# Performance work log

Hardware: AMD Instinct MI355X
Metric: run time of the kernel (lower is better)

## Reference

```python
import jax, jax.numpy as jnp
import numpy as np

NEG = -1e9
NP_N, EP = 30000, 480000
NL, EL, T = 48, 144, 96
NA, D = 11, 256
I_STOP = NL
PHI = 1 + 5 * D + 4 * NA
VAL_VEC = jnp.array([4., 1., 3., 1., 2., 1., 5., 1., 6., 1., 1000.], dtype=jnp.float32)
BOND_VAL = jnp.array([1., 2., 3., 1.5], dtype=jnp.float32)


def gcn2(x, src, dst, w, W1, b1, W2, b2):
    # two-layer GCN with symmetric norm + self loops (PyG GCNConv semantics)
    n = x.shape[0]
    loops = jnp.arange(n, dtype=src.dtype)
    s = jnp.concatenate([src, loops])
    d = jnp.concatenate([dst, loops])
    ww = jnp.concatenate([w, jnp.ones((n,), x.dtype)])
    deg = jax.ops.segment_sum(ww, d, num_segments=n)
    dinv = jnp.where(deg > 0, deg ** -0.5, 0.0)
    norm = (ww * dinv[s] * dinv[d])[:, None]
    def conv(h, W, b):
        return jax.ops.segment_sum((h @ W)[s] * norm, d, num_segments=n) + b
    return conv(jax.nn.relu(conv(x, W1, b1)), W2, b2)


def _forward(x_p, x_l_geom, Wp1, bp1, Wp2, bp2, Wl1, bl1, Wl2, bl2,
             Wd1, bd1, Wd2, bd2, Wf, bf, Wg, bg, Wh, bh,
             src_p, dst_p, src_l, dst_l, x_l_label, bfs_index, bfs_bond):
    f32, i32 = jnp.float32, jnp.int32
    src_p = src_p.astype(i32); dst_p = dst_p.astype(i32)
    src_l = src_l.astype(i32); dst_l = dst_l.astype(i32)
    bfs_index = bfs_index.astype(i32); bfs_bond = bfs_bond.astype(i32)
    x_l_label = x_l_label.astype(i32)
    x_l = jnp.concatenate([x_l_geom, jax.nn.one_hot(x_l_label, NA, dtype=f32)], 1)
    z_pocket = gcn2(x_p, src_p, dst_p, jnp.ones((EP,), f32), Wp1, bp1, Wp2, bp2).mean(0)
    z_l = gcn2(x_l, src_l, dst_l, jnp.ones((EL,), f32), Wl1, bl1, Wl2, bl2)
    lab_true = x_l[:, 4:]
    # f: atom label classifier, teacher-forced log prob of true labels
    lmask = jnp.zeros((NA,), f32).at[-1].set(NEG)
    logp = jax.nn.log_softmax(z_l @ Wf + bf + lmask, -1)[jnp.arange(NL), x_l_label].sum()
    H_init = jnp.concatenate([z_l, lab_true], 1).mean(0)
    lab_v = jnp.concatenate([lab_true, jax.nn.one_hot(jnp.array([NA - 1]), NA, dtype=f32)], 0)  # append Stop node
    e0 = bfs_index[0]
    z_v0 = gcn2(lab_v, e0[:1], e0[1:2], jnp.ones((1,), f32), Wd1, bd1, Wd2, bd2)
    H_t0 = jnp.concatenate([z_v0, lab_v], 1).mean(0)
    val0 = lab_v @ VAL_VEC
    N1 = NL + 1
    E = 2 * T
    Q0 = jnp.zeros((T + 1,), i32).at[0].set(bfs_index[0, 0])
    carry0 = (jnp.asarray(0.0, f32), val0, jnp.zeros((N1,), bool), jnp.zeros((N1, N1), bool),
              jnp.zeros((E,), i32), jnp.zeros((E,), i32), jnp.zeros((E,), bool), jnp.asarray(0, i32),
              Q0, jnp.asarray(0, i32), jnp.asarray(1, i32), z_v0, H_t0, jnp.asarray(0.0, f32))

    def step(carry, xs):
        logp, val, closed, adj, esrc, edst, evalid, ec, Q, head, tail, z_v, H_t, time = carry
        v, bidx = xs
        active = tail > head
        u = Q[head]
        phi = jnp.concatenate([
            jnp.full((N1, 1), time, f32),
            jnp.broadcast_to(z_pocket, (N1, D)),
            jnp.broadcast_to(z_v[u], (N1, D)),
            jnp.broadcast_to(lab_v[u], (N1, NA)),
            z_v, lab_v,
            jnp.broadcast_to(H_t, (N1, D + NA)),
            jnp.broadcast_to(H_init, (N1, D + NA))], 1)
        # node mask (valency / closed / already-bonded / self), then unmask {v, stop}
        base = jnp.where((val < 1) | closed | adj[u], NEG, 0.0).at[u].set(NEG)
        m_nou = jnp.where(val[u] < 1, jnp.full((N1,), NEG, f32), base)
        m = m_nou.at[v].set(0.0).at[I_STOP].set(0.0)
        glog = (phi @ Wg + bg)[:, 0] + m
        logp = logp + jnp.where(active, jax.nn.log_softmax(glog)[v], 0.0)
        is_stop = v == I_STOP
        pop = active & is_stop
        do_edge = active & (~is_stop)
        closed = closed.at[u].set(jnp.where(pop, True, closed[u]))
        head = head + pop.astype(jnp.int32)
        Q = Q.at[tail].set(jnp.where(do_edge, v, Q[tail]), mode='drop')
        tail = tail + do_edge.astype(jnp.int32)
        esrc = esrc.at[ec].set(u, mode='drop').at[ec + 1].set(v, mode='drop')
        edst = edst.at[ec].set(v, mode='drop').at[ec + 1].set(u, mode='drop')
        evalid = evalid.at[ec].set(do_edge, mode='drop').at[ec + 1].set(do_edge, mode='drop')
        ec = ec + 2 * do_edge.astype(jnp.int32)
        # bond mask row on min valency of (u, v)
        mv = jnp.minimum(val[u], val[v])
        two = jnp.array([0., 0., NEG, 0.], f32)
        one = jnp.array([0., NEG, NEG, 0.], f32)
        zer = jnp.full((4,), NEG, f32)
        e = jnp.where(mv <= 2, two, jnp.zeros((4,), f32))
        e = jnp.where(mv <= 1, one, e)
        e = jnp.where(mv <= 0, zer, e)
        e = jnp.where(m_nou[v] <= NEG * 0.5, zer, e)
        e = e.at[bidx].set(0.0)  # unmask true bond
        hlog = phi[v] @ Wh + bh + e
        logp = logp + jnp.where(do_edge, jax.nn.log_softmax(hlog)[bidx], 0.0)
        dec = jnp.where(do_edge, BOND_VAL[bidx], 0.0)
        val = val.at[u].add(-dec).at[v].add(-dec)
        adj = adj.at[u, v].set(jnp.where(do_edge, True, adj[u, v])).at[v, u].set(jnp.where(do_edge, True, adj[v, u]))
        z_new = gcn2(lab_v, esrc, edst, evalid.astype(f32), Wd1, bd1, Wd2, bd2)
        z_v = jnp.where(do_edge, z_new, z_v)
        H_t = jnp.where(do_edge, jnp.concatenate([z_new, lab_v], 1).mean(0), H_t)
        time = time + do_edge.astype(f32)
        return (logp, val, closed, adj, esrc, edst, evalid, ec, Q, head, tail, z_v, H_t, time), None

    carry, _ = jax.lax.scan(step, carry0, (bfs_index[:, 1], bfs_bond))
    return carry[0]


def setup_inputs():
    key = jax.random.key(0)
    ks = jax.random.split(key, 30)
    f32 = jnp.float32
    def w(i, shape):
        return jax.random.normal(ks[i], shape, f32) * 0.05
    inp = {}
    inp['x_p'] = jax.random.normal(ks[0], (NP_N, 15), f32)
    inp['src_p'] = jax.random.randint(ks[1], (EP,), 0, NP_N)
    inp['dst_p'] = jax.random.randint(ks[2], (EP,), 0, NP_N)
    inp['x_l_geom'] = jax.random.normal(ks[3], (NL, 4), f32)
    inp['x_l_label'] = jax.random.randint(ks[4], (NL,), 0, NA - 1)
    inp['src_l'] = jax.random.randint(ks[5], (EL,), 0, NL)
    inp['dst_l'] = jax.random.randint(ks[6], (EL,), 0, NL)
    inp['bfs_index'] = jax.random.randint(ks[7], (T, 2), 0, NL + 1)
    inp['bfs_bond'] = jax.random.randint(ks[8], (T,), 0, 4)
    inp['Wp1'] = w(9, (15, D)); inp['bp1'] = w(10, (D,))
    inp['Wp2'] = w(11, (D, D)); inp['bp2'] = w(12, (D,))
    inp['Wl1'] = w(13, (15, D)); inp['bl1'] = w(14, (D,))
    inp['Wl2'] = w(15, (D, D)); inp['bl2'] = w(16, (D,))
    inp['Wd1'] = w(17, (NA, D)); inp['bd1'] = w(18, (D,))
    inp['Wd2'] = w(19, (D, D)); inp['bd2'] = w(20, (D,))
    inp['Wf'] = w(21, (D, NA)); inp['bf'] = w(22, (NA,))
    inp['Wg'] = w(23, (PHI, 1)); inp['bg'] = w(24, (1,))
    inp['Wh'] = w(25, (PHI, 4)); inp['bh'] = w(26, (4,))
    return inp


def reference(x_p, src_p, dst_p, x_l_geom, x_l_label, src_l, dst_l, bfs_index, bfs_bond,
              Wp1, bp1, Wp2, bp2, Wl1, bl1, Wl2, bl2, Wd1, bd1, Wd2, bd2,
              Wf, bf, Wg, bg, Wh, bh):
    return _forward(x_p, x_l_geom, Wp1, bp1, Wp2, bp2, Wl1, bl1, Wl2, bl2,
                    Wd1, bd1, Wd2, bd2, Wf, bf, Wg, bg, Wh, bh,
                    src_p, dst_p, src_l, dst_l, x_l_label, bfs_index, bfs_bond)
```

## Files before the change

### kernel.cpp

```cpp
#include <hip/hip_runtime.h>
#include <math.h>

#define NPn 30000
#define EPn 480000
#define NLl 48
#define ELl 144
#define Tn 96
#define NAn 11
#define Dn 256
#define N1 49
#define NEGf (-1000000000.0f)
#define NSTATES 97
#define CHN 125
#define PC 13
#define YN (N1*PC)


__global__ __launch_bounds__(256) void kA(
    const int* __restrict__ dst_p, int* __restrict__ deg,
    const int* __restrict__ lab_in, const int* __restrict__ bfs_i, const int* __restrict__ bfs_b,
    int* __restrict__ lab_idx, float* __restrict__ lab_means,
    int* __restrict__ dirs, int* __restrict__ dird, float* __restrict__ m_arr,
    float* __restrict__ e_arr, int* __restrict__ rec, int* __restrict__ Sout,
    const float* __restrict__ xg, const int* __restrict__ srcl, const int* __restrict__ dstl,
    const float* __restrict__ Wl1, const float* __restrict__ bl1,
    const float* __restrict__ Wl2, const float* __restrict__ bl2, float* __restrict__ zl_mean,
    const float* __restrict__ Wd2, const float* __restrict__ Wg, const float* __restrict__ Wh,
    float* __restrict__ Pm){
  const int bid = blockIdx.x;
  const int tid = threadIdx.x;

  if (bid == 0){
    __shared__ int sv[Tn], sb[Tn];
    __shared__ int qarr[Tn+1];
    __shared__ int uArr[Tn], headA[Tn], doeA[Tn], popA[Tn], actA[Tn], timeA[Tn], eidxA[Tn];
    __shared__ float decA[Tn], valuA[Tn], valvA[Tn];
    __shared__ float baseB[Tn][N1];
    __shared__ int slab[N1];
    __shared__ int cntL[NAn];
    if (tid < Tn){ sv[tid]=bfs_i[2*tid+1]; sb[tid]=bfs_b[tid]; }
    if (tid <= Tn) qarr[tid]=0;
    if (tid < NAn) cntL[tid]=0;
    if (tid < N1){ int l=(tid<NLl)? lab_in[tid] : (NAn-1); slab[tid]=l; lab_idx[tid]=l; }
    __syncthreads();
    if (tid < NLl) atomicAdd(&cntL[slab[tid]],1);
    if (tid == 0) qarr[0]=bfs_i[0];
    __syncthreads();
    if (tid < NAn){
      int c=cntL[tid];
      lab_means[tid]     = ((float)c + ((tid==NAn-1)?1.f:0.f))*(1.0f/49.0f);
      lab_means[NAn+tid] = (float)c*(1.0f/48.0f);
    }
    if (tid == 0){
      dirs[192]=qarr[0]; dird[192]=bfs_i[1];
      int head=0, tail=1, ec=0, timec=0;
      for (int t=0;t<Tn;t++){
        int v = sv[t];
        int active = (tail>head)?1:0;
        int is_stop = (v==NLl)?1:0;
        int pop = active & is_stop;
        int doe = active & (is_stop^1);
        headA[t]=head; actA[t]=active; doeA[t]=doe; popA[t]=pop; timeA[t]=timec;
        eidxA[t] = doe ? ec : -1;
        int bix = sb[t];
        decA[t] = (bix==0)?1.f:(bix==1)?2.f:(bix==2)?3.f:1.5f;
        if (doe && tail<=Tn) qarr[tail]=v;
        head+=pop; tail+=doe; ec+=2*doe; timec+=doe;
      }
      Sout[0]=ec/2;
    }
    __syncthreads();
    if (tid < Tn){
      int t=tid;
      int h=headA[t]; if (h>Tn) h=Tn;
      int u=qarr[h];
      uArr[t]=u;
      rec[t]=u; rec[Tn+t]=sv[t]; rec[2*Tn+t]=sb[t];
      rec[3*Tn+t]=actA[t]; rec[4*Tn+t]=doeA[t]; rec[5*Tn+t]=timeA[t];
      int ei=eidxA[t];
      if (ei>=0 && ei<192){
        int v=sv[t];
        dirs[ei]=u; dird[ei]=v; dirs[ei+1]=v; dird[ei+1]=u;
      }
    }
    __syncthreads();
    if (tid < 64){
      const int l = tid;
      int labv = (l<N1)? slab[l] : 0;
      float val;
      switch(labv){
        case 0: val=4.f; break; case 1: val=1.f; break; case 2: val=3.f; break;
        case 3: val=1.f; break; case 4: val=2.f; break; case 5: val=1.f; break;
        case 6: val=5.f; break; case 7: val=1.f; break; case 8: val=6.f; break;
        case 9: val=1.f; break; default: val=1000.f; break;
      }
      if (l>=N1) val=0.f;
      int closed=0;
      unsigned long long adjm=0ull;
      for (int t=0;t<Tn;t++){
        int u=uArr[t], v=sv[t];
        int doe=doeA[t], pop=popA[t];
        float base = (val<1.f || closed || ((adjm>>u)&1ull)) ? NEGf : 0.f;
        if (l==u) base=NEGf;
        if (l<N1) baseB[t][l]=base;
        if (l==u) valuA[t]=val;
        if (l==v) valvA[t]=val;
        if (doe){
          float dec=decA[t];
          if (l==u){ val-=dec; adjm |= (1ull<<v); }
          if (l==v){ val-=dec; adjm |= (1ull<<u); }
        }
        if (pop && l==u) closed=1;
      }
    }
    __syncthreads();
    {
      const int lane=tid&63, wv=tid>>6;
      for (int t=wv; t<Tn; t+=4){
        float valu=valuA[t], valv=valvA[t];
        int v=sv[t], bix=sb[t];
        if (lane<N1){
          float mnou = (valu<1.f)? NEGf : baseB[t][lane];
          float m = mnou;
          if (lane==v) m=0.f;
          if (lane==NLl) m=0.f;
          m_arr[t*N1+lane]=m;
        }
        if (lane<4){
          float mnv = (valu<1.f)? NEGf : baseB[t][v];
          float mv = fminf(valu,valv);
          float e;
          if (mv<=0.f) e=NEGf;
          else if (mv<=1.f) e=((lane==1)||(lane==2))?NEGf:0.f;
          else if (mv<=2.f) e=(lane==2)?NEGf:0.f;
          else e=0.f;
          if (mnv <= NEGf*0.5f) e=NEGf;
          if (lane==bix) e=0.f;
          e_arr[t*4+lane]=e;
        }
      }
    }
    return;
  }

  if (bid == 1){
    __shared__ float sW[15*Dn];
    __shared__ float svec[NLl*4];
    __shared__ float scnt[NLl*11];
    __shared__ float ow[NLl];
    __shared__ float rs[Dn];
    __shared__ float sdinv[NLl];
    __shared__ int sdeg[NLl];
    __shared__ int ses[ELl], sed[ELl];
    __shared__ int slab2[NLl];
    if (tid<NLl){ sdeg[tid]=1; slab2[tid]=lab_in[tid]; }
    for (int i=tid;i<NLl*4;i+=256) svec[i]=0.f;
    for (int i=tid;i<NLl*11;i+=256) scnt[i]=0.f;
    for (int i=tid;i<15*Dn;i+=256) sW[i]=Wl1[i];
    __syncthreads();
    if (tid<ELl){ ses[tid]=srcl[tid]; sed[tid]=dstl[tid]; atomicAdd(&sdeg[dstl[tid]],1); }
    __syncthreads();
    if (tid<NLl) sdinv[tid]=rsqrtf((float)sdeg[tid]);
    __syncthreads();
    if (tid<NLl){
      float dv=sdinv[tid];
      ow[tid]=dv;
      for (int q=0;q<4;q++) svec[tid*4+q]=xg[tid*4+q]*dv;
      scnt[tid*11+slab2[tid]]=dv;
    }
    __syncthreads();
    if (tid<ELl){
      int s=ses[tid], d=sed[tid];
      float dvs=sdinv[s];
      for (int q=0;q<4;q++) atomicAdd(&svec[d*4+q], xg[s*4+q]*dvs);
      atomicAdd(&scnt[d*11+slab2[s]], dvs);
      atomicAdd(&ow[s], sdinv[d]);
    }
    __syncthreads();
    {
      int c=tid;
      float b=bl1[c];
      float rsum=0.f;
      for (int d=0;d<NLl;d++){
        float a=0.f;
        for (int q=0;q<4;q++)  a=fmaf(svec[d*4+q], sW[q*Dn+c], a);
        for (int aa=0;aa<11;aa++) a=fmaf(scnt[d*11+aa], sW[(4+aa)*Dn+c], a);
        float h=fmaxf(sdinv[d]*a + b, 0.f);
        rsum = fmaf(sdinv[d]*ow[d], h, rsum);
      }
      rs[c]=rsum*(1.0f/48.0f);
    }
    __syncthreads();
    {
      int c=tid;
      float a=0.f;
      for (int k=0;k<Dn;k++) a=fmaf(rs[k], Wl2[(size_t)k*Dn+c], a);
      zl_mean[c]=a+bl2[c];
    }
    return;
  }

  if (bid < 2+64){
    const int lane = tid&63, wv = tid>>6;
    const int k = (bid-2)*4 + wv;
    float pg=0.f;
    float4 pu=make_float4(0,0,0,0), pv=make_float4(0,0,0,0), ph=make_float4(0,0,0,0);
    for (int q=0;q<4;q++){
      int n = lane + 64*q;
      float w = Wd2[(size_t)k*Dn+n];
      pg = fmaf(w, Wg[524+n], pg);
      float4 a=*(const float4*)&Wh[(size_t)(257+n)*4];
      float4 b=*(const float4*)&Wh[(size_t)(524+n)*4];
      float4 c=*(const float4*)&Wh[(size_t)(791+n)*4];
      pu.x=fmaf(w,a.x,pu.x); pu.y=fmaf(w,a.y,pu.y); pu.z=fmaf(w,a.z,pu.z); pu.w=fmaf(w,a.w,pu.w);
      pv.x=fmaf(w,b.x,pv.x); pv.y=fmaf(w,b.y,pv.y); pv.z=fmaf(w,b.z,pv.z); pv.w=fmaf(w,b.w,pv.w);
      ph.x=fmaf(w,c.x,ph.x); ph.y=fmaf(w,c.y,ph.y); ph.z=fmaf(w,c.z,ph.z); ph.w=fmaf(w,c.w,ph.w);
    }
    for (int off=32; off>0; off>>=1){
      pg += __shfl_xor(pg,off);
      pu.x+=__shfl_xor(pu.x,off); pu.y+=__shfl_xor(pu.y,off); pu.z+=__shfl_xor(pu.z,off); pu.w+=__shfl_xor(pu.w,off);
      pv.x+=__shfl_xor(pv.x,off); pv.y+=__shfl_xor(pv.y,off); pv.z+=__shfl_xor(pv.z,off); pv.w+=__shfl_xor(pv.w,off);
      ph.x+=__shfl_xor(ph.x,off); ph.y+=__shfl_xor(ph.y,off); ph.z+=__shfl_xor(ph.z,off); ph.w+=__shfl_xor(ph.w,off);
    }
    if (lane==0){
      float* o = Pm + k*PC;
      o[0]=pg; o[1]=pu.x; o[2]=pu.y; o[3]=pu.z; o[4]=pu.w;
      o[5]=pv.x; o[6]=pv.y; o[7]=pv.z; o[8]=pv.w;
      o[9]=ph.x; o[10]=ph.y; o[11]=ph.z; o[12]=ph.w;
    }
    return;
  }

  {
    int e = (bid-66)*256 + tid;
    if (e < EPn) atomicAdd(&deg[dst_p[e]], 1);
  }
}


__global__ void k_xagg(const int* __restrict__ src, const int* __restrict__ dst,
                       const float* __restrict__ xp, const int* __restrict__ deg,
                       float* __restrict__ xagg, float* __restrict__ odegw){
  int g = blockIdx.x*blockDim.x + threadIdx.x;
  int e = g>>4, c = g&15;
  if (e >= EPn) return;
  int s = src[e], d = dst[e];
  if (c < 15){
    float dvs = rsqrtf((float)(deg[s]+1));
    atomicAdd(&xagg[d*16+c], xp[s*15+c]*dvs);
  } else {
    float dvd = rsqrtf((float)(deg[d]+1));
    atomicAdd(&odegw[s], dvd);
  }
}

__global__ __launch_bounds__(256) void k_fuse(const float* __restrict__ xp, const float* __restrict__ xagg,
    const int* __restrict__ deg, const float* __restrict__ odegw,
    const float* __restrict__ Wp1, const float* __restrict__ bp1, float* __restrict__ zr){
  __shared__ float sx[CHN][16];
  __shared__ float sc[CHN];
  int tid = threadIdx.x;
  int base = blockIdx.x*CHN;
  float wcol[15];
  for (int k=0;k<15;k++) wcol[k]=Wp1[k*Dn+tid];
  float b = bp1[tid];
  for (int i=tid;i<CHN*16;i+=256){
    int n = base+(i>>4), c = i&15;
    float v = 0.f;
    if (n<NPn && c<15){
      float dv = rsqrtf((float)(deg[n]+1));
      v = (xagg[n*16+c] + xp[n*15+c]*dv)*dv;
    }
    sx[i>>4][i&15]=v;
  }
  for (int i=tid;i<CHN;i+=256){
    int n = base+i;
    float dv = (n<NPn)? rsqrtf((float)(deg[n]+1)) : 0.f;
    sc[i] = (n<NPn)? dv*(odegw[n]+dv) : 0.f;
  }
  __syncthreads();
  float acc = 0.f;
  int lim = (NPn-base < CHN)? (NPn-base) : CHN;
  for (int i=0;i<lim;i++){
    float d0 = b;
    for (int k=0;k<15;k++) d0 = fmaf(sx[i][k], wcol[k], d0);
    acc = fmaf(sc[i], fmaxf(d0,0.f), acc);
  }
  atomicAdd(&zr[tid], acc);
}


__global__ __launch_bounds__(256) void k_zh(const float* __restrict__ zr, const float* __restrict__ Wp2,
    const float* __restrict__ bp2, const float* __restrict__ zl, const float* __restrict__ lm,
    const float* __restrict__ b2, const float* __restrict__ Wh, const float* __restrict__ bh,
    float* __restrict__ hc4){
  __shared__ float sr[Dn];
  __shared__ float zp[Dn];
  int tid=threadIdx.x;
  sr[tid]=zr[tid]*(1.0f/30000.0f);
  __syncthreads();
  float a=0.f;
  for (int k=0;k<Dn;k++) a=fmaf(sr[k],Wp2[(size_t)k*Dn+tid],a);
  zp[tid]=a+bp2[tid];
  __syncthreads();
  if (tid<64){
    int lane=tid;
    float4 h=make_float4(0,0,0,0);
    for (int q=0;q<4;q++){
      int n=lane+64*q;
      float4 w1=*(const float4*)&Wh[(size_t)(1+n)*4];
      float4 w2=*(const float4*)&Wh[(size_t)(1058+n)*4];
      float4 wu=*(const float4*)&Wh[(size_t)(257+n)*4];
      float4 wv=*(const float4*)&Wh[(size_t)(524+n)*4];
      float4 wh=*(const float4*)&Wh[(size_t)(791+n)*4];
      float zpn=zp[n], zln=zl[n], bn=b2[n];
      h.x += zpn*w1.x + zln*w2.x + bn*(wu.x+wv.x+wh.x);
      h.y += zpn*w1.y + zln*w2.y + bn*(wu.y+wv.y+wh.y);
      h.z += zpn*w1.z + zln*w2.z + bn*(wu.z+wv.z+wh.z);
      h.w += zpn*w1.w + zln*w2.w + bn*(wu.w+wv.w+wh.w);
    }
    if (lane<NAn){
      float4 wa=*(const float4*)&Wh[(size_t)(1047+lane)*4];
      float4 wb=*(const float4*)&Wh[(size_t)(1314+lane)*4];
      float aa=lm[lane], bb=lm[NAn+lane];
      h.x += aa*wa.x + bb*wb.x; h.y += aa*wa.y + bb*wb.y;
      h.z += aa*wa.z + bb*wb.z; h.w += aa*wa.w + bb*wb.w;
    }
    for (int off=32; off>0; off>>=1){
      h.x+=__shfl_xor(h.x,off); h.y+=__shfl_xor(h.y,off);
      h.z+=__shfl_xor(h.z,off); h.w+=__shfl_xor(h.w,off);
    }
    if (lane==0){
      hc4[0]=h.x+bh[0]; hc4[1]=h.y+bh[1]; hc4[2]=h.z+bh[2]; hc4[3]=h.w+bh[3];
    }
  }
}


__global__ __launch_bounds__(256) void k_dc(const int* __restrict__ Sp, const int* __restrict__ dirs,
    const int* __restrict__ dird, const int* __restrict__ lab_idx,
    const float* __restrict__ Wd1, const float* __restrict__ bd1,
    const float* __restrict__ Pm, const int* __restrict__ rec,
    const float* __restrict__ m_arr, const float* __restrict__ e_arr,
    const float* __restrict__ hc4, const float* __restrict__ Wg, const float* __restrict__ Wh,
    float* __restrict__ out){
  int k = blockIdx.x;
  if (k > Sp[0]) return;
  __shared__ float sW[11*Dn];
  __shared__ float sP[Dn*PC];
  __shared__ float hT[Dn*N1];
  __shared__ float cnt[N1*11];
  __shared__ float y1[YN];
  __shared__ float za[YN];
  __shared__ float sdinv[N1];
  __shared__ int sdeg[N1];
  __shared__ int se[192], sd[192];
  __shared__ int slab[N1];
  __shared__ int srec[6*Tn];
  int tid=threadIdx.x;
  int ecnt = (k==0)?1:(2*k);
  int base = (k==0)?192:0;
  if (tid<N1){ sdeg[tid]=1; slab[tid]=lab_idx[tid]; }
  for (int i=tid;i<N1*11;i+=256) cnt[i]=0.f;
  for (int i=tid;i<11*Dn;i+=256) sW[i]=Wd1[i];
  for (int i=tid;i<Dn*PC;i+=256) sP[i]=Pm[i];
  for (int i=tid;i<6*Tn;i+=256) srec[i]=rec[i];
  __syncthreads();
  if (tid<ecnt){ se[tid]=dirs[base+tid]; sd[tid]=dird[base+tid]; atomicAdd(&sdeg[sd[tid]],1); }
  __syncthreads();
  if (tid<N1) sdinv[tid]=rsqrtf((float)sdeg[tid]);
  __syncthreads();
  if (tid<N1) cnt[tid*11+slab[tid]] = sdinv[tid];
  __syncthreads();
  if (tid<ecnt) atomicAdd(&cnt[sd[tid]*11+slab[se[tid]]], sdinv[se[tid]]);
  __syncthreads();
  {
    int c=tid;
    float wreg[11];
    for (int a=0;a<11;a++) wreg[a]=sW[a*Dn+c];
    float b=bd1[c];
    for (int r=0;r<N1;r++){
      float s=0.f;
      for (int a=0;a<11;a++) s=fmaf(cnt[r*11+a], wreg[a], s);
      hT[c*N1+r]=fmaxf(sdinv[r]*s + b, 0.f);
    }
  }
  __syncthreads();
  for (int idx=tid; idx<YN; idx+=256){
    int r=idx/PC, j=idx-r*PC;
    float acc=0.f;
    for (int c=0;c<Dn;c++) acc=fmaf(hT[c*N1+r], sP[c*PC+j], acc);
    y1[idx]=acc;
    za[idx]=sdinv[r]*acc;
  }
  __syncthreads();
  for (int i=tid; i<ecnt*PC; i+=256){
    int e=i/PC, j=i-e*PC;
    atomicAdd(&za[sd[e]*PC+j], sdinv[se[e]]*y1[se[e]*PC+j]);
  }
  __syncthreads();
  for (int idx=tid; idx<YN; idx+=256){
    int r=idx/PC;
    za[idx]=sdinv[r]*za[idx];
  }
  __syncthreads();
  if (tid>=64) return;
  const int lane=tid;
  for (int t=0;t<Tn;t++){
    if (!srec[3*Tn+t] || srec[5*Tn+t]!=k) continue;
    const int u=srec[t], v=srec[Tn+t], bidx=srec[2*Tn+t], doe=srec[4*Tn+t];
    float g = -INFINITY;
    float4 hm = make_float4(0,0,0,0);
    if (lane<N1){
      const float* zrow = za + lane*PC;
      g = zrow[0] + Wg[780+slab[lane]] + m_arr[t*N1+lane];
      hm.x=zrow[9]; hm.y=zrow[10]; hm.z=zrow[11]; hm.w=zrow[12];
    }
    float gv = __shfl(g, v);
    float gM = g;
    for (int off=32; off>0; off>>=1) gM = fmaxf(gM, __shfl_xor(gM, off));
    float ex = (lane<N1)? expf(g-gM) : 0.f;
    float gS = ex;
    for (int off=32; off>0; off>>=1){
      gS += __shfl_xor(gS, off);
      hm.x+=__shfl_xor(hm.x,off); hm.y+=__shfl_xor(hm.y,off);
      hm.z+=__shfl_xor(hm.z,off); hm.w+=__shfl_xor(hm.w,off);
    }
    if (lane==0){
      float res = gv - gM - logf(gS);
      if (doe){
        const int lu=slab[u], lv=slab[v];
        const float tf=(float)k;
        float h[4];
        for (int j=0;j<4;j++){
          float hmj = (j==0)?hm.x:(j==1)?hm.y:(j==2)?hm.z:hm.w;
          h[j] = hc4[j] + tf*Wh[j] + Wh[(513+lu)*4+j] + Wh[(780+lv)*4+j]
               + za[u*PC+1+j] + za[v*PC+5+j] + hmj*(1.0f/49.0f) + e_arr[4*t+j];
        }
        float M=fmaxf(fmaxf(h[0],h[1]),fmaxf(h[2],h[3]));
        float se2=expf(h[0]-M)+expf(h[1]-M)+expf(h[2]-M)+expf(h[3]-M);
        float hb=(bidx==0)?h[0]:(bidx==1)?h[1]:(bidx==2)?h[2]:h[3];
        res += hb - M - logf(se2);
      }
      atomicAdd(out, res);
    }
  }
}


extern "C" void kernel_launch(void* const* d_in, const int* in_sizes, int n_in,
                              void* d_out, int out_size, void* d_ws, size_t ws_size,
                              hipStream_t stream){
  const float* x_p      =(const float*)d_in[0];
  const int*   src_p    =(const int*)d_in[1];
  const int*   dst_p    =(const int*)d_in[2];
  const float* x_l_geom =(const float*)d_in[3];
  const int*   x_l_label=(const int*)d_in[4];
  const int*   src_l    =(const int*)d_in[5];
  const int*   dst_l    =(const int*)d_in[6];
  const int*   bfs_index=(const int*)d_in[7];
  const int*   bfs_bond =(const int*)d_in[8];
  const float* Wp1=(const float*)d_in[9];
  const float* bp1=(const float*)d_in[10];
  const float* Wp2=(const float*)d_in[11];
  const float* bp2=(const float*)d_in[12];
  const float* Wl1=(const float*)d_in[13];
  const float* bl1=(const float*)d_in[14];
  const float* Wl2=(const float*)d_in[15];
  const float* bl2=(const float*)d_in[16];
  const float* Wd1=(const float*)d_in[17];
  const float* bd1=(const float*)d_in[18];
  const float* Wd2=(const float*)d_in[19];
  const float* bd2=(const float*)d_in[20];
  const float* Wg =(const float*)d_in[23];
  const float* Wh =(const float*)d_in[25];
  const float* bh =(const float*)d_in[26];

  char* w=(char*)d_ws;
  size_t off=0;
  auto alloc=[&](size_t bytes)->char*{ char* p=w+off; off=(off+bytes+255)&~((size_t)255); return p; };
  int*   deg    =(int*)alloc((size_t)NPn*4);
  float* odegw  =(float*)alloc((size_t)NPn*4);
  float* xagg   =(float*)alloc((size_t)NPn*16*4);
  float* zr     =(float*)alloc(Dn*4);
  size_t zero_span = off;
  float* zl_mean=(float*)alloc(Dn*4);
  float* Pm     =(float*)alloc(Dn*PC*4);
  float* hc4    =(float*)alloc(4*4);
  float* m_arr  =(float*)alloc((size_t)Tn*N1*4);
  float* e_arr  =(float*)alloc((size_t)Tn*4*4);
  int*   rec    =(int*)alloc((size_t)6*Tn*4);
  int*   dirs   =(int*)alloc(194*4);
  int*   dird   =(int*)alloc(194*4);
  int*   lab_idx=(int*)alloc(N1*4);
  float* lab_means=(float*)alloc(2*NAn*4);
  int*   Sval   =(int*)alloc(4);
  (void)in_sizes;(void)n_in;(void)ws_size;

  hipMemsetAsync(d_ws, 0, zero_span, stream);
  hipMemsetAsync(d_out, 0, (size_t)out_size*sizeof(float), stream);

  kA<<<66 + EPn/256, 256, 0, stream>>>(
      dst_p, deg,
      x_l_label, bfs_index, bfs_bond, lab_idx, lab_means, dirs, dird, m_arr, e_arr, rec, Sval,
      x_l_geom, src_l, dst_l, Wl1, bl1, Wl2, bl2, zl_mean,
      Wd2, Wg, Wh, Pm);
  k_xagg<<<EPn*16/256,256,0,stream>>>(src_p,dst_p,x_p,deg,xagg,odegw);
  k_fuse<<<(NPn+CHN-1)/CHN,256,0,stream>>>(x_p,xagg,deg,odegw,Wp1,bp1,zr);
  k_zh<<<1,256,0,stream>>>(zr,Wp2,bp2,zl_mean,lab_means,bd2,Wh,bh,hc4);
  k_dc<<<NSTATES,256,0,stream>>>(Sval,dirs,dird,lab_idx,Wd1,bd1,Pm,rec,m_arr,e_arr,hc4,Wg,Wh,(float*)d_out);
}
```

Baseline: 273.5 us.

## Replace atomic scatter of pocket features with CSR build and gather aggregation

Replaces the per-edge, per-channel atomic scatter into xagg with a CSR build. A prefix scan over in-degrees produces row pointers, a fill kernel places source indices with a cursor atomic, and k_fuse then gathers pre-scaled 16-wide rows with float4 loads. This cuts the atomic traffic from sixteen per edge to two per edge, at the cost of two extra kernel launches, a single-block scan and non-deterministic neighbor ordering within rows. It also packs the BFS control state into int2 in block 0 and vectorises the ligand layer-1 aggregation in block 1.

Result: slower. 316.9 us (+15.8%).

```diff
diff --git a/kernel.cpp b/kernel.cpp
--- a/kernel.cpp
+++ b/kernel.cpp
@@ -33,8 +33,8 @@
   if (bid == 0){
     __shared__ int sv[Tn], sb[Tn];
     __shared__ int qarr[Tn+1];
-    __shared__ int uArr[Tn], headA[Tn], doeA[Tn], popA[Tn], actA[Tn], timeA[Tn], eidxA[Tn];
-    __shared__ float decA[Tn], valuA[Tn], valvA[Tn];
+    __shared__ int2 ctrl[Tn];
+    __shared__ float valuA[Tn], valvA[Tn];
     __shared__ float baseB[Tn][N1];
     __shared__ int slab[N1];
     __shared__ int cntL[NAn];
@@ -55,38 +55,32 @@
       dirs[192]=qarr[0]; dird[192]=bfs_i[1];
       int head=0, tail=1, ec=0, timec=0;
       for (int t=0;t<Tn;t++){
-        int v = sv[t];
+        int v = sv[t], bix = sb[t];
         int active = (tail>head)?1:0;
+        int h = (head<=Tn)? head : Tn;
+        int u = qarr[h];
         int is_stop = (v==NLl)?1:0;
         int pop = active & is_stop;
         int doe = active & (is_stop^1);
-        headA[t]=head; actA[t]=active; doeA[t]=doe; popA[t]=pop; timeA[t]=timec;
-        eidxA[t] = doe ? ec : -1;
-        int bix = sb[t];
-        decA[t] = (bix==0)?1.f:(bix==1)?2.f:(bix==2)?3.f:1.5f;
-        if (doe && tail<=Tn) qarr[tail]=v;
+        ctrl[t] = make_int2(u | (doe<<8) | (pop<<9) | (active<<10) | (timec<<16), v | (bix<<8));
+        if (doe){
+          if (tail<=Tn) qarr[tail]=v;
+          if (ec<192){ dirs[ec]=u; dird[ec]=v; dirs[ec+1]=v; dird[ec+1]=u; }
+        }
         head+=pop; tail+=doe; ec+=2*doe; timec+=doe;
       }
       Sout[0]=ec/2;
     }
     __syncthreads();
     if (tid < Tn){
-      int t=tid;
-      int h=headA[t]; if (h>Tn) h=Tn;
-      int u=qarr[h];
-      uArr[t]=u;
-      rec[t]=u; rec[Tn+t]=sv[t]; rec[2*Tn+t]=sb[t];
-      rec[3*Tn+t]=actA[t]; rec[4*Tn+t]=doeA[t]; rec[5*Tn+t]=timeA[t];
-      int ei=eidxA[t];
-      if (ei>=0 && ei<192){
-        int v=sv[t];
-        dirs[ei]=u; dird[ei]=v; dirs[ei+1]=v; dird[ei+1]=u;
-      }
+      int2 c=ctrl[tid];
+      rec[tid]=c.x&255; rec[Tn+tid]=c.y&255; rec[2*Tn+tid]=(c.y>>8)&3;
+      rec[3*Tn+tid]=(c.x>>10)&1; rec[4*Tn+tid]=(c.x>>8)&1; rec[5*Tn+tid]=(c.x>>16)&255;
     }
     __syncthreads();
     if (tid < 64){
       const int l = tid;
-      int labv = (l<N1)? slab[l] : 0;
+      int labv = (l<N1)? slab[l] : (NAn-1);
       float val;
       switch(labv){
         case 0: val=4.f; break; case 1: val=1.f; break; case 2: val=3.f; break;
@@ -97,16 +91,18 @@
       if (l>=N1) val=0.f;
       int closed=0;
       unsigned long long adjm=0ull;
+      #pragma unroll 4
       for (int t=0;t<Tn;t++){
-        int u=uArr[t], v=sv[t];
-        int doe=doeA[t], pop=popA[t];
+        int2 c=ctrl[t];
+        int u=c.x&255, doe=(c.x>>8)&1, pop=(c.x>>9)&1;
+        int v=c.y&255, bix=(c.y>>8)&3;
         float base = (val<1.f || closed || ((adjm>>u)&1ull)) ? NEGf : 0.f;
         if (l==u) base=NEGf;
         if (l<N1) baseB[t][l]=base;
         if (l==u) valuA[t]=val;
         if (l==v) valvA[t]=val;
         if (doe){
-          float dec=decA[t];
+          float dec = (bix==0)?1.f:(bix==1)?2.f:(bix==2)?3.f:1.5f;
           if (l==u){ val-=dec; adjm |= (1ull<<v); }
           if (l==v){ val-=dec; adjm |= (1ull<<u); }
         }
@@ -145,8 +141,7 @@
 
   if (bid == 1){
     __shared__ float sW[15*Dn];
-    __shared__ float svec[NLl*4];
-    __shared__ float scnt[NLl*11];
+    __shared__ __align__(16) float sagg[NLl][16];
     __shared__ float ow[NLl];
     __shared__ float rs[Dn];
     __shared__ float sdinv[NLl];
@@ -154,8 +149,7 @@
     __shared__ int ses[ELl], sed[ELl];
     __shared__ int slab2[NLl];
     if (tid<NLl){ sdeg[tid]=1; slab2[tid]=lab_in[tid]; }
-    for (int i=tid;i<NLl*4;i+=256) svec[i]=0.f;
-    for (int i=tid;i<NLl*11;i+=256) scnt[i]=0.f;
+    for (int i=tid;i<NLl*16;i+=256) sagg[i>>4][i&15]=0.f;
     for (int i=tid;i<15*Dn;i+=256) sW[i]=Wl1[i];
     __syncthreads();
     if (tid<ELl){ ses[tid]=srcl[tid]; sed[tid]=dstl[tid]; atomicAdd(&sdeg[dstl[tid]],1); }
@@ -165,26 +159,34 @@
     if (tid<NLl){
       float dv=sdinv[tid];
       ow[tid]=dv;
-      for (int q=0;q<4;q++) svec[tid*4+q]=xg[tid*4+q]*dv;
-      scnt[tid*11+slab2[tid]]=dv;
+      for (int q=0;q<4;q++) sagg[tid][q]=xg[tid*4+q]*dv;
+      sagg[tid][4+slab2[tid]]=dv;
     }
     __syncthreads();
     if (tid<ELl){
       int s=ses[tid], d=sed[tid];
       float dvs=sdinv[s];
-      for (int q=0;q<4;q++) atomicAdd(&svec[d*4+q], xg[s*4+q]*dvs);
-      atomicAdd(&scnt[d*11+slab2[s]], dvs);
+      for (int q=0;q<4;q++) atomicAdd(&sagg[d][q], xg[s*4+q]*dvs);
+      atomicAdd(&sagg[d][4+slab2[s]], dvs);
       atomicAdd(&ow[s], sdinv[d]);
     }
     __syncthreads();
     {
       int c=tid;
+      float wcol[16];
+      #pragma unroll
+      for (int q=0;q<15;q++) wcol[q]=sW[q*Dn+c];
+      wcol[15]=0.f;
       float b=bl1[c];
       float rsum=0.f;
       for (int d=0;d<NLl;d++){
+        const float4* ar=(const float4*)sagg[d];
+        float4 x0=ar[0],x1=ar[1],x2=ar[2],x3=ar[3];
         float a=0.f;
-        for (int q=0;q<4;q++)  a=fmaf(svec[d*4+q], sW[q*Dn+c], a);
-        for (int aa=0;aa<11;aa++) a=fmaf(scnt[d*11+aa], sW[(4+aa)*Dn+c], a);
+        a=fmaf(x0.x,wcol[0],a); a=fmaf(x0.y,wcol[1],a); a=fmaf(x0.z,wcol[2],a); a=fmaf(x0.w,wcol[3],a);
+        a=fmaf(x1.x,wcol[4],a); a=fmaf(x1.y,wcol[5],a); a=fmaf(x1.z,wcol[6],a); a=fmaf(x1.w,wcol[7],a);
+        a=fmaf(x2.x,wcol[8],a); a=fmaf(x2.y,wcol[9],a); a=fmaf(x2.z,wcol[10],a); a=fmaf(x2.w,wcol[11],a);
+        a=fmaf(x3.x,wcol[12],a); a=fmaf(x3.y,wcol[13],a); a=fmaf(x3.z,wcol[14],a);
         float h=fmaxf(sdinv[d]*a + b, 0.f);
         rsum = fmaf(sdinv[d]*ow[d], h, rsum);
       }
@@ -238,52 +240,104 @@
 }
 
 
-__global__ void k_xagg(const int* __restrict__ src, const int* __restrict__ dst,
-                       const float* __restrict__ xp, const int* __restrict__ deg,
-                       float* __restrict__ xagg, float* __restrict__ odegw){
-  int g = blockIdx.x*blockDim.x + threadIdx.x;
-  int e = g>>4, c = g&15;
+__global__ __launch_bounds__(1024) void k_prep(const int* __restrict__ deg, const float* __restrict__ xp,
+    int* __restrict__ rowptr, int* __restrict__ cursor, float* __restrict__ xp16){
+  if (blockIdx.x == 0){
+    __shared__ int part[1024];
+    const int t = threadIdx.x;
+    const int base = t*30;
+    int loc[30];
+    int s=0;
+    #pragma unroll
+    for (int i=0;i<30;i++){
+      int idx=base+i;
+      int v=(idx<NPn)? deg[idx] : 0;
+      loc[i]=s; s+=v;
+    }
+    part[t]=s;
+    __syncthreads();
+    for (int off=1; off<1024; off<<=1){
+      int x = (t>=off)? part[t-off] : 0;
+      __syncthreads();
+      part[t]+=x;
+      __syncthreads();
+    }
+    int excl = part[t]-s;
+    #pragma unroll
+    for (int i=0;i<30;i++){
+      int idx=base+i;
+      if (idx<NPn){ int rp=excl+loc[i]; rowptr[idx]=rp; cursor[idx]=rp; }
+    }
+    if (t==1023) rowptr[NPn]=part[1023];
+    return;
+  }
+  int r = (blockIdx.x-1)*64 + (threadIdx.x>>4), c = threadIdx.x&15;
+  if (r < NPn){
+    float dv = rsqrtf((float)(deg[r]+1));
+    float v = (c<15)? xp[r*15+c]*dv : dv;
+    xp16[(size_t)r*16+c]=v;
+  }
+}
+
+
+__global__ void k_fill(const int* __restrict__ src, const int* __restrict__ dst,
+                       const int* __restrict__ deg, int* __restrict__ cursor,
+                       int* __restrict__ colidx, float* __restrict__ odegw){
+  int e = blockIdx.x*blockDim.x + threadIdx.x;
   if (e >= EPn) return;
   int s = src[e], d = dst[e];
-  if (c < 15){
-    float dvs = rsqrtf((float)(deg[s]+1));
-    atomicAdd(&xagg[d*16+c], xp[s*15+c]*dvs);
-  } else {
-    float dvd = rsqrtf((float)(deg[d]+1));
-    atomicAdd(&odegw[s], dvd);
-  }
-}
-
-__global__ __launch_bounds__(256) void k_fuse(const float* __restrict__ xp, const float* __restrict__ xagg,
+  atomicAdd(&odegw[s], rsqrtf((float)(deg[d]+1)));
+  int pos = atomicAdd(&cursor[d], 1);
+  colidx[pos] = s;
+}
+
+
+__global__ __launch_bounds__(256) void k_fuse(const float* __restrict__ xp16,
     const int* __restrict__ deg, const float* __restrict__ odegw,
+    const int* __restrict__ rowptr, const int* __restrict__ colidx,
     const float* __restrict__ Wp1, const float* __restrict__ bp1, float* __restrict__ zr){
-  __shared__ float sx[CHN][16];
+  __shared__ __align__(16) float sx[CHN][16];
   __shared__ float sc[CHN];
-  int tid = threadIdx.x;
-  int base = blockIdx.x*CHN;
-  float wcol[15];
+  const int tid = threadIdx.x;
+  const int base = blockIdx.x*CHN;
+  if (tid < CHN){
+    int n = base + tid;
+    const float4* xr = (const float4*)(xp16 + (size_t)n*16);
+    float4 a0=xr[0], a1=xr[1], a2=xr[2], a3=xr[3];
+    int e0=rowptr[n], e1=rowptr[n+1];
+    for (int e=e0;e<e1;e++){
+      int s=colidx[e];
+      const float4* xs=(const float4*)(xp16 + (size_t)s*16);
+      float4 b0=xs[0], b1=xs[1], b2=xs[2], b3=xs[3];
+      a0.x+=b0.x; a0.y+=b0.y; a0.z+=b0.z; a0.w+=b0.w;
+      a1.x+=b1.x; a1.y+=b1.y; a1.z+=b1.z; a1.w+=b1.w;
+      a2.x+=b2.x; a2.y+=b2.y; a2.z+=b2.z; a2.w+=b2.w;
+      a3.x+=b3.x; a3.y+=b3.y; a3.z+=b3.z; a3.w+=b3.w;
+    }
+    float dv = rsqrtf((float)(deg[n]+1));
+    a0.x*=dv; a0.y*=dv; a0.z*=dv; a0.w*=dv;
+    a1.x*=dv; a1.y*=dv; a1.z*=dv; a1.w*=dv;
+    a2.x*=dv; a2.y*=dv; a2.z*=dv; a2.w*=dv;
+    a3.x*=dv; a3.y*=dv; a3.z*=dv; a3.w*=dv;
+    float4* so=(float4*)sx[tid];
+    so[0]=a0; so[1]=a1; so[2]=a2; so[3]=a3;
+    sc[tid]=dv*(odegw[n]+dv);
+  }
+  __syncthreads();
+  float wcol[16];
+  #pragma unroll
   for (int k=0;k<15;k++) wcol[k]=Wp1[k*Dn+tid];
+  wcol[15]=0.f;
   float b = bp1[tid];
-  for (int i=tid;i<CHN*16;i+=256){
-    int n = base+(i>>4), c = i&15;
-    float v = 0.f;
-    if (n<NPn && c<15){
-      float dv = rsqrtf((float)(deg[n]+1));
-      v = (xagg[n*16+c] + xp[n*15+c]*dv)*dv;
-    }
-    sx[i>>4][i&15]=v;
-  }
-  for (int i=tid;i<CHN;i+=256){
-    int n = base+i;
-    float dv = (n<NPn)? rsqrtf((float)(deg[n]+1)) : 0.f;
-    sc[i] = (n<NPn)? dv*(odegw[n]+dv) : 0.f;
-  }
-  __syncthreads();
   float acc = 0.f;
-  int lim = (NPn-base < CHN)? (NPn-base) : CHN;
-  for (int i=0;i<lim;i++){
-    float d0 = b;
-    for (int k=0;k<15;k++) d0 = fmaf(sx[i][k], wcol[k], d0);
+  for (int i=0;i<CHN;i++){
+    const float4* sr=(const float4*)sx[i];
+    float4 x0=sr[0],x1=sr[1],x2=sr[2],x3=sr[3];
+    float d0=b;
+    d0=fmaf(x0.x,wcol[0],d0); d0=fmaf(x0.y,wcol[1],d0); d0=fmaf(x0.z,wcol[2],d0); d0=fmaf(x0.w,wcol[3],d0);
+    d0=fmaf(x1.x,wcol[4],d0); d0=fmaf(x1.y,wcol[5],d0); d0=fmaf(x1.z,wcol[6],d0); d0=fmaf(x1.w,wcol[7],d0);
+    d0=fmaf(x2.x,wcol[8],d0); d0=fmaf(x2.y,wcol[9],d0); d0=fmaf(x2.z,wcol[10],d0); d0=fmaf(x2.w,wcol[11],d0);
+    d0=fmaf(x3.x,wcol[12],d0); d0=fmaf(x3.y,wcol[13],d0); d0=fmaf(x3.z,wcol[14],d0);
     acc = fmaf(sc[i], fmaxf(d0,0.f), acc);
   }
   atomicAdd(&zr[tid], acc);
@@ -481,9 +535,12 @@
   auto alloc=[&](size_t bytes)->char*{ char* p=w+off; off=(off+bytes+255)&~((size_t)255); return p; };
   int*   deg    =(int*)alloc((size_t)NPn*4);
   float* odegw  =(float*)alloc((size_t)NPn*4);
-  float* xagg   =(float*)alloc((size_t)NPn*16*4);
   float* zr     =(float*)alloc(Dn*4);
   size_t zero_span = off;
+  int*   rowptr =(int*)alloc((size_t)(NPn+1)*4);
+  int*   cursor =(int*)alloc((size_t)NPn*4);
+  int*   colidx =(int*)alloc((size_t)EPn*4);
+  float* xp16   =(float*)alloc((size_t)NPn*16*4);
   float* zl_mean=(float*)alloc(Dn*4);
   float* Pm     =(float*)alloc(Dn*PC*4);
   float* hc4    =(float*)alloc(4*4);
@@ -505,8 +562,9 @@
       x_l_label, bfs_index, bfs_bond, lab_idx, lab_means, dirs, dird, m_arr, e_arr, rec, Sval,
       x_l_geom, src_l, dst_l, Wl1, bl1, Wl2, bl2, zl_mean,
       Wd2, Wg, Wh, Pm);
-  k_xagg<<<EPn*16/256,256,0,stream>>>(src_p,dst_p,x_p,deg,xagg,odegw);
-  k_fuse<<<(NPn+CHN-1)/CHN,256,0,stream>>>(x_p,xagg,deg,odegw,Wp1,bp1,zr);
+  k_prep<<<1 + (NPn+63)/64, 1024, 0, stream>>>(deg, x_p, rowptr, cursor, xp16);
+  k_fill<<<(EPn+255)/256, 256, 0, stream>>>(src_p, dst_p, deg, cursor, colidx, odegw);
+  k_fuse<<<NPn/CHN, 256, 0, stream>>>(xp16, deg, odegw, rowptr, colidx, Wp1, bp1, zr);
   k_zh<<<1,256,0,stream>>>(zr,Wp2,bp2,zl_mean,lab_means,bd2,Wh,bh,hc4);
   k_dc<<<NSTATES,256,0,stream>>>(Sval,dirs,dird,lab_idx,Wd1,bd1,Pm,rec,m_arr,e_arr,hc4,Wg,Wh,(float*)d_out);
 }
```
